# Optimization experiments

Measured on AMD Instinct MI355X. Metric: run time of the kernel, lower is better.

## Reference

```python
import jax, jax.numpy as jnp
import numpy as np

B, S, DM, H, FF, BLOCK, R = 2, 4096, 768, 12, 3072, 64, 3
NB = S // BLOCK  # 64 blocks


def _layer_norm(x, g, b, eps=1e-5):
    mu = jnp.mean(x, -1, keepdims=True)
    var = jnp.var(x, -1, keepdims=True)
    return (x - mu) * jax.lax.rsqrt(var + eps) * g + b


def _bigbird_attn(x, rand_attn, Wq, bq, Wk, bk, Wv, bv):
    b_, s_, dm = x.shape
    h_ = H
    d = dm // h_
    n = s_ // BLOCK
    r = rand_attn.shape[-1]
    scale = 1.0 / np.sqrt(d).astype(np.float32)

    def heads(y):  # [B,S,DM] -> [B,H,n,block,D]
        return y.reshape(b_, s_, h_, d).transpose(0, 2, 1, 3).reshape(b_, h_, n, BLOCK, d)

    qb = heads(x @ Wq + bq)
    kb = heads(x @ Wk + bk)
    vb = heads(x @ Wv + bv)
    k_full = kb.reshape(b_, h_, s_, d)
    v_full = vb.reshape(b_, h_, s_, d)

    # gather random key/value blocks per head: [B,H,n-2,r*block,D]
    gather = jax.vmap(lambda zh, idx: zh[:, idx], in_axes=(1, 0), out_axes=1)
    gk = gather(kb, rand_attn).reshape(b_, h_, n - 2, r * BLOCK, d)
    gv = gather(vb, rand_attn).reshape(b_, h_, n - 2, r * BLOCK, d)

    def attend(q, k, v):
        s = jnp.einsum('...qd,...kd->...qk', q, k) * scale
        a = jax.nn.softmax(s, axis=-1)
        return jnp.einsum('...qk,...kd->...qd', a, v)

    # first block: full attention over all keys
    c_first = attend(qb[:, :, 0], k_full, v_full)

    # second block: blocks 0,1,2 + last block + random blocks
    k2 = jnp.concatenate([kb[:, :, 0], kb[:, :, 1], kb[:, :, 2], kb[:, :, -1], gk[:, :, 0]], axis=2)
    v2 = jnp.concatenate([vb[:, :, 0], vb[:, :, 1], vb[:, :, 2], vb[:, :, -1], gv[:, :, 0]], axis=2)
    c_second = attend(qb[:, :, 1], k2, v2)

    # middle blocks 2..n-3: global-first + 3-block sliding window + random + global-last
    m = n - 4
    qm = qb[:, :, 2:-2]  # [B,H,m,block,D]

    def band(z):  # sliding window of 3 blocks around each middle block
        return jnp.concatenate([z[:, :, 1:-3], z[:, :, 2:-2], z[:, :, 3:-1]], axis=3)

    bc = lambda z: jnp.broadcast_to(z[:, :, None], (b_, h_, m, BLOCK, d))
    km = jnp.concatenate([bc(kb[:, :, 0]), band(kb), gk[:, :, 1:-1], bc(kb[:, :, -1])], axis=3)
    vm = jnp.concatenate([bc(vb[:, :, 0]), band(vb), gv[:, :, 1:-1], bc(vb[:, :, -1])], axis=3)
    c_mid = attend(qm, km, vm)  # [B,H,m,block,D]

    # second-to-last block: block 0 + last three blocks + random blocks
    kp = jnp.concatenate([kb[:, :, 0], kb[:, :, -3], kb[:, :, -2], kb[:, :, -1], gk[:, :, -1]], axis=2)
    vp = jnp.concatenate([vb[:, :, 0], vb[:, :, -3], vb[:, :, -2], vb[:, :, -1], gv[:, :, -1]], axis=2)
    c_pen = attend(qb[:, :, -2], kp, vp)

    # last block: full attention over all keys
    c_last = attend(qb[:, :, -1], k_full, v_full)

    ctx = jnp.concatenate([c_first[:, :, None], c_second[:, :, None], c_mid,
                           c_pen[:, :, None], c_last[:, :, None]], axis=2)
    return ctx.reshape(b_, h_, s_, d).transpose(0, 2, 1, 3).reshape(b_, s_, dm)


def setup_inputs() -> dict:
    key = jax.random.key(0)
    ks = jax.random.split(key, 16)
    p = lambda k, shape: (jax.random.normal(k, shape, jnp.float32) * 0.02)
    return {
        'x': jax.random.normal(ks[0], (B, S, DM), jnp.float32),
        'rand_attn': jax.random.randint(ks[1], (H, NB - 2, R), 0, NB - 2, jnp.int32),
        'Wq': p(ks[2], (DM, DM)), 'bq': jnp.zeros((DM,), jnp.float32),
        'Wk': p(ks[3], (DM, DM)), 'bk': jnp.zeros((DM,), jnp.float32),
        'Wv': p(ks[4], (DM, DM)), 'bv': jnp.zeros((DM,), jnp.float32),
        'ln1_g': jnp.ones((DM,), jnp.float32), 'ln1_b': jnp.zeros((DM,), jnp.float32),
        'W1': p(ks[5], (DM, FF)), 'b1': jnp.zeros((FF,), jnp.float32),
        'W2': p(ks[6], (FF, DM)), 'b2': jnp.zeros((DM,), jnp.float32),
        'ln2_g': jnp.ones((DM,), jnp.float32), 'ln2_b': jnp.zeros((DM,), jnp.float32),
    }


def reference(x, rand_attn, Wq, bq, Wk, bk, Wv, bv, ln1_g, ln1_b, W1, b1, W2, b2, ln2_g, ln2_b):
    attn = _bigbird_attn(x, rand_attn, Wq, bq, Wk, bk, Wv, bv)
    h = _layer_norm(attn + x, ln1_g, ln1_b)  # dropout is identity in eval
    ffn = jax.nn.gelu(h @ W1 + b1, approximate=False) @ W2 + b2
    return _layer_norm(ffn + h, ln2_g, ln2_b)
```

## Files before the change

### kernel.cpp

```cpp
#include <hip/hip_runtime.h>
#include <cmath>


typedef unsigned short bf;
typedef __attribute__((ext_vector_type(8))) short bf16x8;
typedef __attribute__((ext_vector_type(4))) float f32x4;

__device__ __forceinline__ float bf2f(bf u) { return __uint_as_float(((unsigned)u) << 16); }
__device__ __forceinline__ bf f2bf(float f) {
  unsigned x = __float_as_uint(f);
  x += 0x7FFFu + ((x >> 16) & 1u);
  return (bf)(x >> 16);
}

__device__ __forceinline__ void gload16(const bf* g, char* lds) {
  __builtin_amdgcn_global_load_lds(
      (const __attribute__((address_space(1))) void*)g,
      (__attribute__((address_space(3))) void*)lds, 16, 0, 0);
}

__global__ __launch_bounds__(256) void cvt_x_k(const float* __restrict__ X,
                                               bf* __restrict__ xb)
{
  size_t i = ((size_t)blockIdx.x * 256 + threadIdx.x) * 8;
  float4 f0 = *(const float4*)&X[i];
  float4 f1 = *(const float4*)&X[i + 4];
  *(ushort4*)&xb[i]     = make_ushort4(f2bf(f0.x), f2bf(f0.y), f2bf(f0.z), f2bf(f0.w));
  *(ushort4*)&xb[i + 4] = make_ushort4(f2bf(f1.x), f2bf(f1.y), f2bf(f1.z), f2bf(f1.w));
}

__global__ __launch_bounds__(256) void tconv_k(const float* __restrict__ W,
                                               bf* __restrict__ Wt, int K, int N)
{
  __shared__ float tile[64][65];
  const int t = threadIdx.x;
  const int bn = blockIdx.x * 64, bk = blockIdx.y * 64;
  const int r = t >> 2, c0 = (t & 3) * 16;
  #pragma unroll
  for (int i = 0; i < 4; ++i) {
    float4 f = *(const float4*)&W[(size_t)(bk + r) * N + bn + c0 + i * 4];
    tile[r][c0 + i*4 + 0] = f.x; tile[r][c0 + i*4 + 1] = f.y;
    tile[r][c0 + i*4 + 2] = f.z; tile[r][c0 + i*4 + 3] = f.w;
  }
  __syncthreads();
  #pragma unroll
  for (int i = 0; i < 4; ++i) {
    int c = c0 + i * 4;
    ushort4 u = make_ushort4(f2bf(tile[c + 0][r]), f2bf(tile[c + 1][r]),
                             f2bf(tile[c + 2][r]), f2bf(tile[c + 3][r]));
    *(ushort4*)&Wt[(size_t)(bn + r) * K + bk + c] = u;
  }
}

__global__ __launch_bounds__(256) void tconv3_k(const float* __restrict__ Wq,
                                                const float* __restrict__ Wk,
                                                const float* __restrict__ Wv,
                                                bf* __restrict__ Wt)
{
  __shared__ float tile[64][65];
  const float* W = (blockIdx.z == 0) ? Wq : ((blockIdx.z == 1) ? Wk : Wv);
  bf* dst = Wt + (size_t)blockIdx.z * 589824;
  const int t = threadIdx.x;
  const int bn = blockIdx.x * 64, bk = blockIdx.y * 64;
  const int r = t >> 2, c0 = (t & 3) * 16;
  #pragma unroll
  for (int i = 0; i < 4; ++i) {
    float4 f = *(const float4*)&W[(size_t)(bk + r) * 768 + bn + c0 + i * 4];
    tile[r][c0 + i*4 + 0] = f.x; tile[r][c0 + i*4 + 1] = f.y;
    tile[r][c0 + i*4 + 2] = f.z; tile[r][c0 + i*4 + 3] = f.w;
  }
  __syncthreads();
  #pragma unroll
  for (int i = 0; i < 4; ++i) {
    int c = c0 + i * 4;
    ushort4 u = make_ushort4(f2bf(tile[c + 0][r]), f2bf(tile[c + 1][r]),
                             f2bf(tile[c + 2][r]), f2bf(tile[c + 3][r]));
    *(ushort4*)&dst[(size_t)(bn + r) * 768 + bk + c] = u;
  }
}

template <int BN, typename TC>
__global__ __launch_bounds__(256) void gl_gemm_k(
    const bf* __restrict__ A, const bf* __restrict__ Bt,
    const float* __restrict__ bias, TC* __restrict__ C,
    int M, int N, int K, int ldbt, int ep)
{
  constexpr int NJ = BN / 32;
  constexpr int ASZ = 16384;
  constexpr int BSZ = BN * 128;
  __shared__ char smem[2 * (ASZ + BSZ)];
  const int t = threadIdx.x;
  const int bm = blockIdx.y * 128, bn = blockIdx.x * BN;
  const int lane = t & 63, wid = t >> 6;
  const int wm = wid >> 1, wn = wid & 1;
  const int fr = lane & 15, fq = lane >> 4;
  const int lr = lane >> 3;
  const int lksw = (((lane & 7) ^ lr) << 3);

  f32x4 acc[4][NJ];
  #pragma unroll
  for (int i = 0; i < 4; ++i)
    #pragma unroll
    for (int j = 0; j < NJ; ++j) acc[i][j] = (f32x4){0.f, 0.f, 0.f, 0.f};

  auto STAGE = [&](int p, int k0) {
    char* sA = smem + p * (ASZ + BSZ);
    char* sB = sA + ASZ;
    #pragma unroll
    for (int c = 0; c < 4; ++c) {
      int chunk = wid * 4 + c;
      gload16(A + (size_t)(bm + chunk * 8 + lr) * K + k0 + lksw, sA + chunk * 1024);
    }
    #pragma unroll
    for (int c = 0; c < NJ; ++c) {
      int chunk = wid * NJ + c;
      gload16(Bt + (size_t)(bn + chunk * 8 + lr) * ldbt + k0 + lksw, sB + chunk * 1024);
    }
  };

  const int T = K >> 6;
  STAGE(0, 0);
  asm volatile("s_waitcnt vmcnt(0)" ::: "memory");
  __builtin_amdgcn_s_barrier();
  __builtin_amdgcn_sched_barrier(0);
  int cur = 0;
  for (int tt = 0; tt < T; ++tt) {
    if (tt + 1 < T) STAGE(cur ^ 1, (tt + 1) * 64);
    __builtin_amdgcn_sched_barrier(0);
    char* sA = smem + cur * (ASZ + BSZ);
    char* sB = sA + ASZ;
    __builtin_amdgcn_s_setprio(1);
    #pragma unroll
    for (int kk = 0; kk < 2; ++kk) {
      const int kb = kk * 64 + fq * 16;
      bf16x8 a[4], b[NJ];
      #pragma unroll
      for (int i = 0; i < 4; ++i) {
        int row = wm * 64 + i * 16 + fr;
        a[i] = *(const bf16x8*)(sA + row * 128 + (kb ^ ((row & 7) << 4)));
      }
      #pragma unroll
      for (int j = 0; j < NJ; ++j) {
        int col = wn * (BN / 2) + j * 16 + fr;
        b[j] = *(const bf16x8*)(sB + col * 128 + (kb ^ ((col & 7) << 4)));
      }
      #pragma unroll
      for (int i = 0; i < 4; ++i)
        #pragma unroll
        for (int j = 0; j < NJ; ++j)
          acc[i][j] = __builtin_amdgcn_mfma_f32_16x16x32_bf16(a[i], b[j], acc[i][j], 0, 0, 0);
    }
    __builtin_amdgcn_s_setprio(0);
    __builtin_amdgcn_sched_barrier(0);
    asm volatile("s_waitcnt vmcnt(0)" ::: "memory");
    __builtin_amdgcn_s_barrier();
    __builtin_amdgcn_sched_barrier(0);
    cur ^= 1;
  }
  #pragma unroll
  for (int j = 0; j < NJ; ++j) {
    int col = bn + wn * (BN / 2) + j * 16 + fr;
    float bias_v = bias ? bias[col] : 0.f;
    #pragma unroll
    for (int i = 0; i < 4; ++i) {
      int row0 = bm + wm * 64 + i * 16 + fq * 4;
      #pragma unroll
      for (int r = 0; r < 4; ++r) {
        float v = acc[i][j][r] + bias_v;
        if (ep == 1) v = 0.5f * v * (1.0f + erff(v * 0.70710678118654752f));
        if constexpr (sizeof(TC) == 2) C[(size_t)(row0 + r) * N + col] = f2bf(v);
        else                           C[(size_t)(row0 + r) * N + col] = v;
      }
    }
  }
}

__global__ __launch_bounds__(256) void qkv_gl_k(
    const bf* __restrict__ A, const bf* __restrict__ Bt,
    const float* __restrict__ bq, const float* __restrict__ bk,
    const float* __restrict__ bv,
    bf* __restrict__ Qo, bf* __restrict__ Ko, bf* __restrict__ Vo)
{
  constexpr int ASZ = 16384, BSZ = 16384;
  __shared__ char smem[2 * (ASZ + BSZ)];
  const int t = threadIdx.x;
  const int bm = blockIdx.y * 128, bn = blockIdx.x * 128;
  const int lane = t & 63, wid = t >> 6;
  const int wm = wid >> 1, wn = wid & 1;
  const int fr = lane & 15, fq = lane >> 4;
  const int lr = lane >> 3;
  const int lksw = (((lane & 7) ^ lr) << 3);
  const int K = 768;

  f32x4 acc[4][4];
  #pragma unroll
  for (int i = 0; i < 4; ++i)
    #pragma unroll
    for (int j = 0; j < 4; ++j) acc[i][j] = (f32x4){0.f, 0.f, 0.f, 0.f};

  auto STAGE = [&](int p, int k0) {
    char* sA = smem + p * (ASZ + BSZ);
    char* sB = sA + ASZ;
    #pragma unroll
    for (int c = 0; c < 4; ++c) {
      int chunk = wid * 4 + c;
      gload16(A + (size_t)(bm + chunk * 8 + lr) * K + k0 + lksw, sA + chunk * 1024);
    }
    #pragma unroll
    for (int c = 0; c < 4; ++c) {
      int chunk = wid * 4 + c;
      gload16(Bt + (size_t)(bn + chunk * 8 + lr) * K + k0 + lksw, sB + chunk * 1024);
    }
  };

  STAGE(0, 0);
  asm volatile("s_waitcnt vmcnt(0)" ::: "memory");
  __builtin_amdgcn_s_barrier();
  __builtin_amdgcn_sched_barrier(0);
  int cur = 0;
  for (int tt = 0; tt < 12; ++tt) {
    if (tt + 1 < 12) STAGE(cur ^ 1, (tt + 1) * 64);
    __builtin_amdgcn_sched_barrier(0);
    char* sA = smem + cur * (ASZ + BSZ);
    char* sB = sA + ASZ;
    __builtin_amdgcn_s_setprio(1);
    #pragma unroll
    for (int kk = 0; kk < 2; ++kk) {
      const int kb = kk * 64 + fq * 16;
      bf16x8 a[4], b[4];
      #pragma unroll
      for (int i = 0; i < 4; ++i) {
        int row = wm * 64 + i * 16 + fr;
        a[i] = *(const bf16x8*)(sA + row * 128 + (kb ^ ((row & 7) << 4)));
      }
      #pragma unroll
      for (int j = 0; j < 4; ++j) {
        int col = wn * 64 + j * 16 + fr;
        b[j] = *(const bf16x8*)(sB + col * 128 + (kb ^ ((col & 7) << 4)));
      }
      #pragma unroll
      for (int i = 0; i < 4; ++i)
        #pragma unroll
        for (int j = 0; j < 4; ++j)
          acc[i][j] = __builtin_amdgcn_mfma_f32_16x16x32_bf16(a[i], b[j], acc[i][j], 0, 0, 0);
    }
    __builtin_amdgcn_s_setprio(0);
    __builtin_amdgcn_sched_barrier(0);
    asm volatile("s_waitcnt vmcnt(0)" ::: "memory");
    __builtin_amdgcn_s_barrier();
    __builtin_amdgcn_sched_barrier(0);
    cur ^= 1;
  }
  const int seg = bn / 768;
  const int cb  = bn - seg * 768;
  bf* dst = (seg == 0) ? Qo : ((seg == 1) ? Ko : Vo);
  const float* bias = (seg == 0) ? bq : ((seg == 1) ? bk : bv);
  #pragma unroll
  for (int j = 0; j < 4; ++j) {
    int col = cb + wn * 64 + j * 16 + fr;
    float bias_v = bias[col];
    #pragma unroll
    for (int i = 0; i < 4; ++i) {
      int row0 = bm + wm * 64 + i * 16 + fq * 4;
      #pragma unroll
      for (int r = 0; r < 4; ++r)
        dst[(size_t)(row0 + r) * 768 + col] = f2bf(acc[i][j][r] + bias_v);
    }
  }
}

__device__ __forceinline__ void stage_kv(char* bK, char* bVT,
    int kkey, int kd0, int vkey, int w,
    uint4 k0, uint4 k1, uint4 v0, uint4 v1)
{
  const int sw = (kkey & 7) << 4;
  *(uint4*)(bK + kkey * 128 + ((2 * kd0) ^ sw))      = k0;
  *(uint4*)(bK + kkey * 128 + ((2 * kd0 + 16) ^ sw)) = k1;
  union { uint4 q; unsigned short s[8]; } a, c;
  a.q = v0; c.q = v1;
  #pragma unroll
  for (int i = 0; i < 8; ++i) {
    int d = w * 16 + i;
    *(unsigned short*)(bVT + d * 128 + ((2 * vkey) ^ ((d & 7) << 4))) = a.s[i];
  }
  #pragma unroll
  for (int i = 0; i < 8; ++i) {
    int d = w * 16 + 8 + i;
    *(unsigned short*)(bVT + d * 128 + ((2 * vkey) ^ ((d & 7) << 4))) = c.s[i];
  }
}

__global__ __launch_bounds__(256) void attn5_kernel(
    const bf* __restrict__ Q, const bf* __restrict__ K,
    const bf* __restrict__ V, const int* __restrict__ rnd,
    float* __restrict__ ctx, float* __restrict__ part, int nseg)
{
  __shared__ char sQP[8192];
  __shared__ char sKV[2][16384];
  __shared__ int klist[8];
  const int t = threadIdx.x;
  const int lane = t & 63, w = t >> 6;
  const int fr = lane & 15, fq = lane >> 4;
  const int wg = blockIdx.x;
  const int nheavy = 48 * nseg;
  const bool heavy = wg < nheavy;
  int b, h, n, nkb, seg = 0, hidx = 0, segBase = 0;
  if (heavy) {
    hidx = wg / nseg; seg = wg - hidx * nseg;
    n = (hidx & 1) ? 63 : 0;
    int bh = hidx >> 1; h = bh % 12; b = bh / 12;
    nkb = 64 / nseg; segBase = seg * nkb;
  } else {
    int idx = wg - nheavy;
    n = 1 + (idx % 62);
    int bh = idx / 62; h = bh % 12; b = bh / 12;
    nkb = (n == 1 || n == 62) ? 7 : 8;
    if (t == 0) {
      int cnt = 0;
      if (n == 1)       { klist[0]=0; klist[1]=1;  klist[2]=2;  klist[3]=63; cnt=4; }
      else if (n == 62) { klist[0]=0; klist[1]=61; klist[2]=62; klist[3]=63; cnt=4; }
      else              { klist[0]=0; klist[1]=n-1; klist[2]=n; klist[3]=n+1; cnt=4; }
      for (int j = 0; j < 3; ++j) klist[cnt++] = rnd[(h * 62 + (n - 1)) * 3 + j];
      if (n != 1 && n != 62) klist[cnt++] = 63;
    }
  }
  const size_t qbase = ((size_t)b * 4096 + (size_t)n * 64) * 768 + h * 64;

  {
    int row = t >> 2, d0 = (t & 3) * 16;
    const bf* qp = &Q[qbase + (size_t)row * 768 + d0];
    #pragma unroll
    for (int i = 0; i < 2; ++i) {
      int off = row * 128 + ((2 * (d0 + 8 * i)) ^ ((row & 7) << 4));
      *(uint4*)(sQP + off) = *(const uint4*)(qp + 8 * i);
    }
  }
  __syncthreads();
  bf16x8 qf[2];
  {
    int row = w * 16 + fr;
    qf[0] = *(const bf16x8*)(sQP + row * 128 + ((2 * (fq * 8))      ^ ((row & 7) << 4)));
    qf[1] = *(const bf16x8*)(sQP + row * 128 + ((2 * (32 + fq * 8)) ^ ((row & 7) << 4)));
  }

  const int kkey = t >> 2, kd0 = (t & 3) * 16;
  const int vkey = lane;

  uint4 pk0, pk1, pv0, pv1;
  {
    int kb = heavy ? segBase : klist[0];
    size_t kbase = ((size_t)b * 4096 + (size_t)kb * 64) * 768 + h * 64;
    const bf* kp = &K[kbase + (size_t)kkey * 768 + kd0];
    pk0 = *(const uint4*)kp;  pk1 = *(const uint4*)(kp + 8);
    const bf* vp = &V[kbase + (size_t)vkey * 768 + w * 16];
    pv0 = *(const uint4*)vp;  pv1 = *(const uint4*)(vp + 8);
  }
  stage_kv(sKV[0], sKV[0] + 8192, kkey, kd0, vkey, w, pk0, pk1, pv0, pv1);

  float m_r[4] = {-1e30f, -1e30f, -1e30f, -1e30f};
  float l_r[4] = {0.f, 0.f, 0.f, 0.f};
  f32x4 acc_o[4];
  #pragma unroll
  for (int j = 0; j < 4; ++j) acc_o[j] = (f32x4){0.f, 0.f, 0.f, 0.f};

  for (int ib = 0; ib < nkb; ++ib) {
    char* bK  = sKV[ib & 1];
    char* bVT = bK + 8192;
    const bool pfv = (ib + 1 < nkb);
    if (pfv) {
      int kb = heavy ? (segBase + ib + 1) : klist[ib + 1];
      size_t kbase = ((size_t)b * 4096 + (size_t)kb * 64) * 768 + h * 64;
      const bf* kp = &K[kbase + (size_t)kkey * 768 + kd0];
      pk0 = *(const uint4*)kp;  pk1 = *(const uint4*)(kp + 8);
      const bf* vp = &V[kbase + (size_t)vkey * 768 + w * 16];
      pv0 = *(const uint4*)vp;  pv1 = *(const uint4*)(vp + 8);
    }
    __syncthreads();
    f32x4 s4[4];
    #pragma unroll
    for (int j = 0; j < 4; ++j) s4[j] = (f32x4){0.f, 0.f, 0.f, 0.f};
    __builtin_amdgcn_s_setprio(1);
    #pragma unroll
    for (int kk = 0; kk < 2; ++kk) {
      #pragma unroll
      for (int j = 0; j < 4; ++j) {
        int key = j * 16 + fr;
        bf16x8 kf = *(const bf16x8*)(bK + key * 128 + ((2 * (kk * 32 + fq * 8)) ^ ((key & 7) << 4)));
        s4[j] = __builtin_amdgcn_mfma_f32_16x16x32_bf16(qf[kk], kf, s4[j], 0, 0, 0);
      }
    }
    __builtin_amdgcn_s_setprio(0);
    #pragma unroll
    for (int j = 0; j < 4; ++j) s4[j] *= 0.125f;
    float c_r[4];
    #pragma unroll
    for (int r = 0; r < 4; ++r) {
      float mx = fmaxf(fmaxf(s4[0][r], s4[1][r]), fmaxf(s4[2][r], s4[3][r]));
      #pragma unroll
      for (int m = 1; m < 16; m <<= 1) mx = fmaxf(mx, __shfl_xor(mx, m, 64));
      float mn = fmaxf(mx, m_r[r]);
      float c  = __expf(m_r[r] - mn);
      float p0 = __expf(s4[0][r] - mn), p1 = __expf(s4[1][r] - mn);
      float p2 = __expf(s4[2][r] - mn), p3 = __expf(s4[3][r] - mn);
      s4[0][r] = p0; s4[1][r] = p1; s4[2][r] = p2; s4[3][r] = p3;
      float sum = p0 + p1 + p2 + p3;
      #pragma unroll
      for (int m = 1; m < 16; m <<= 1) sum += __shfl_xor(sum, m, 64);
      l_r[r] = l_r[r] * c + sum;
      m_r[r] = mn;
      c_r[r] = c;
    }
    #pragma unroll
    for (int j = 0; j < 4; ++j)
      #pragma unroll
      for (int r = 0; r < 4; ++r) acc_o[j][r] *= c_r[r];
    #pragma unroll
    for (int r = 0; r < 4; ++r) {
      int prow = w * 16 + fq * 4 + r;
      int rs = prow * 128, sw = (prow & 7) << 4;
      #pragma unroll
      for (int j = 0; j < 4; ++j)
        *(unsigned short*)(sQP + rs + ((2 * (j * 16 + fr)) ^ sw)) = f2bf(s4[j][r]);
    }
    if (pfv)
      stage_kv(sKV[(ib & 1) ^ 1], sKV[(ib & 1) ^ 1] + 8192, kkey, kd0, vkey, w,
               pk0, pk1, pv0, pv1);
    __builtin_amdgcn_s_setprio(1);
    #pragma unroll
    for (int kk = 0; kk < 2; ++kk) {
      int prow = w * 16 + fr;
      bf16x8 pf8 = *(const bf16x8*)(sQP + prow * 128 + ((2 * (kk * 32 + fq * 8)) ^ ((prow & 7) << 4)));
      #pragma unroll
      for (int j = 0; j < 4; ++j) {
        int col = j * 16 + fr;
        bf16x8 vf = *(const bf16x8*)(bVT + col * 128 + ((2 * (kk * 32 + fq * 8)) ^ ((col & 7) << 4)));
        acc_o[j] = __builtin_amdgcn_mfma_f32_16x16x32_bf16(pf8, vf, acc_o[j], 0, 0, 0);
      }
    }
    __builtin_amdgcn_s_setprio(0);
  }
  if (heavy && nseg > 1) {
    float* pb = part + ((size_t)hidx * nseg + seg) * 4224;
    int row0 = w * 16 + fq * 4;
    #pragma unroll
    for (int r = 0; r < 4; ++r) {
      int row = row0 + r;
      if (fr == 0) { pb[4096 + row] = m_r[r]; pb[4160 + row] = l_r[r]; }
      #pragma unroll
      for (int j = 0; j < 4; ++j)
        pb[row * 64 + j * 16 + fr] = acc_o[j][r];
    }
  } else {
    int row0 = w * 16 + fq * 4;
    #pragma unroll
    for (int r = 0; r < 4; ++r) {
      float inv = 1.f / l_r[r];
      size_t rowoff = qbase + (size_t)(row0 + r) * 768;
      #pragma unroll
      for (int j = 0; j < 4; ++j)
        ctx[rowoff + j * 16 + fr] = acc_o[j][r] * inv;
    }
  }
}

__global__ __launch_bounds__(256) void attn_combine_k(
    const float* __restrict__ part, float* __restrict__ ctx)
{
  const int hidx = blockIdx.x;
  const int t = threadIdx.x;
  const int n = (hidx & 1) ? 63 : 0;
  const int bh = hidx >> 1;
  const int h = bh % 12, b = bh / 12;
  const size_t qbase = ((size_t)b * 4096 + (size_t)n * 64) * 768 + h * 64;
  const int r = t >> 2, d0 = (t & 3) * 16;
  const float* pb = part + (size_t)hidx * 8 * 4224;
  float mi[8], li[8], m = -1e30f;
  #pragma unroll
  for (int i = 0; i < 8; ++i) {
    mi[i] = pb[i * 4224 + 4096 + r];
    li[i] = pb[i * 4224 + 4160 + r];
    m = fmaxf(m, mi[i]);
  }
  float w8[8], L = 0.f;
  #pragma unroll
  for (int i = 0; i < 8; ++i) { w8[i] = __expf(mi[i] - m); L += li[i] * w8[i]; }
  float inv = 1.f / L;
  #pragma unroll
  for (int dd = 0; dd < 4; ++dd) {
    int d = d0 + dd * 4;
    float4 o = {0.f, 0.f, 0.f, 0.f};
    #pragma unroll
    for (int i = 0; i < 8; ++i) {
      float4 p = *(const float4*)&pb[i * 4224 + r * 64 + d];
      o.x = fmaf(w8[i], p.x, o.x); o.y = fmaf(w8[i], p.y, o.y);
      o.z = fmaf(w8[i], p.z, o.z); o.w = fmaf(w8[i], p.w, o.w);
    }
    o.x *= inv; o.y *= inv; o.z *= inv; o.w *= inv;
    *(float4*)&ctx[qbase + (size_t)r * 768 + d] = o;
  }
}

template <typename TR, typename TO>
__global__ __launch_bounds__(256) void ln_kernel(
    const float* __restrict__ a, const TR* __restrict__ res,
    const float* __restrict__ g, const float* __restrict__ bb,
    TO* __restrict__ out)
{
  const int row = blockIdx.x, t = threadIdx.x;
  __shared__ float buf[768];
  __shared__ float rs[4], rss[4];
  const size_t base = (size_t)row * 768;
  float s = 0.f, ss = 0.f;
  for (int c = t; c < 768; c += 256) {
    float rv;
    if constexpr (sizeof(TR) == 2) rv = bf2f(res[base + c]);
    else                           rv = res[base + c];
    float v = a[base + c] + rv;
    buf[c] = v;
    s += v;
    ss = fmaf(v, v, ss);
  }
  #pragma unroll
  for (int off = 32; off > 0; off >>= 1) {
    s  += __shfl_down(s, off, 64);
    ss += __shfl_down(ss, off, 64);
  }
  if ((t & 63) == 0) { rs[t >> 6] = s; rss[t >> 6] = ss; }
  __syncthreads();
  float S  = rs[0] + rs[1] + rs[2] + rs[3];
  float SS = rss[0] + rss[1] + rss[2] + rss[3];
  float mu  = S * (1.f / 768.f);
  float var = SS * (1.f / 768.f) - mu * mu;
  float inv = rsqrtf(var + 1e-5f);
  for (int c = t; c < 768; c += 256) {
    float v = (buf[c] - mu) * inv * g[c] + bb[c];
    if constexpr (sizeof(TO) == 2) out[base + c] = f2bf(v);
    else                           out[base + c] = v;
  }
}

extern "C" void kernel_launch(void* const* d_in, const int* in_sizes, int n_in,
                              void* d_out, int out_size, void* d_ws, size_t ws_size,
                              hipStream_t stream)
{
  const float* x   = (const float*)d_in[0];
  const int*   rnd = (const int*)d_in[1];
  const float* Wq  = (const float*)d_in[2];
  const float* bq  = (const float*)d_in[3];
  const float* Wk  = (const float*)d_in[4];
  const float* bk  = (const float*)d_in[5];
  const float* Wv  = (const float*)d_in[6];
  const float* bv  = (const float*)d_in[7];
  const float* g1  = (const float*)d_in[8];
  const float* be1 = (const float*)d_in[9];
  const float* W1  = (const float*)d_in[10];
  const float* b1  = (const float*)d_in[11];
  const float* W2  = (const float*)d_in[12];
  const float* b2  = (const float*)d_in[13];
  const float* g2  = (const float*)d_in[14];
  const float* be2 = (const float*)d_in[15];
  float* out = (float*)d_out;

  char* W = (char*)d_ws;
  bf* w1t   = (bf*)(W);
  bf* w2t   = (bf*)(W + 4718592);
  bf* Kb    = (bf*)(W + 9437184);
  bf* wqkv  = (bf*)(W + 22020096);
  bf* xb    = (bf*)(W + 25559040);
  bf* Qb    = (bf*)(W + 38141952);
  bf* Vb    = (bf*)(W + 50724864);
  float* part = (float*)(W + 63307776);
  bf* f1    = (bf*)(W + 22020096);
  bf* h1    = Kb;
  float* ctx = out;
  float* f2  = out;

  dim3 blk(256);
  cvt_x_k<<<dim3(3072), blk, 0, stream>>>(x, xb);
  tconv3_k<<<dim3(12, 12, 3), blk, 0, stream>>>(Wq, Wk, Wv, wqkv);
  tconv_k<<<dim3(48, 12), blk, 0, stream>>>(W1, w1t,  768, 3072);
  tconv_k<<<dim3(12, 48), blk, 0, stream>>>(W2, w2t, 3072,  768);
  qkv_gl_k<<<dim3(18, 64), blk, 0, stream>>>(xb, wqkv, bq, bk, bv, Qb, Kb, Vb);
  attn5_kernel<<<dim3(48 * 8 + 2 * 12 * 62), blk, 0, stream>>>(
      Qb, Kb, Vb, rnd, ctx, part, 8);
  attn_combine_k<<<dim3(48), blk, 0, stream>>>(part, ctx);
  ln_kernel<float, bf><<<dim3(8192), blk, 0, stream>>>(ctx, x, g1, be1, h1);
  gl_gemm_k<128, bf><<<dim3(24, 64), blk, 0, stream>>>(
      h1, w1t, b1, f1, 8192, 3072, 768, 768, 1);
  gl_gemm_k<128, float><<<dim3(6, 64), blk, 0, stream>>>(
      f1, w2t, b2, f2, 8192, 768, 3072, 3072, 0);
  ln_kernel<bf, float><<<dim3(8192), blk, 0, stream>>>(f2, h1, g2, be2, out);
}
```

Baseline: 280.3 us.

## Add 256x256-tile 8-wave pipelined GEMM for FFN up-projection with fused GELU

Replaces the 128x128-tile GEMM for the first FFN matmul with a new kernel that uses 512 threads and 256x256 output tiles. It double-buffers 64-wide K slices in 128 KB of LDS, staged in half-tile pieces interleaved with MFMA work under explicit vmcnt waits and barriers. The larger tile raises operand reuse per LDS byte and overlaps global loads with compute, and the epilogue keeps the bias and erf GELU. The cost is heavy register and LDS use, so only one block fits per CU, and the grid shrinks to 384 blocks, which may not fill every CU evenly.

```diff
diff --git a/kernel.cpp b/kernel.cpp
--- a/kernel.cpp
+++ b/kernel.cpp
@@ -76,6 +76,116 @@
     ushort4 u = make_ushort4(f2bf(tile[c + 0][r]), f2bf(tile[c + 1][r]),
                              f2bf(tile[c + 2][r]), f2bf(tile[c + 3][r]));
     *(ushort4*)&dst[(size_t)(bn + r) * 768 + bk + c] = u;
+  }
+}
+
+__global__ __launch_bounds__(512) void gemm8_k(
+    const bf* __restrict__ A, const bf* __restrict__ Bt,
+    const float* __restrict__ bias, bf* __restrict__ C,
+    int M, int N, int K, int ldbt)
+{
+  __shared__ char smem[131072];
+  const int t = threadIdx.x;
+  const int bm = blockIdx.y * 256, bn = blockIdx.x * 256;
+  const int lane = t & 63, wid = t >> 6;
+  const int wm = wid >> 2, wn = wid & 3;
+  const int fr = lane & 15, fq = lane >> 4;
+
+  f32x4 acc[8][4];
+  #pragma unroll
+  for (int i = 0; i < 8; ++i)
+    #pragma unroll
+    for (int q = 0; q < 4; ++q) acc[i][q] = (f32x4){0.f, 0.f, 0.f, 0.f};
+
+  auto STAGE_HALF = [&](int d, int which, int kt) {
+    char* base = smem + d * 65536 + ((which >= 2) ? 32768 : 0);
+    int h = which & 1;
+    const bf* P = (which >= 2) ? Bt : A;
+    int ld  = (which >= 2) ? ldbt : K;
+    int rc0 = ((which >= 2) ? bn : bm) + h * 128;
+    int k0  = kt * 64;
+    #pragma unroll
+    for (int c = 0; c < 2; ++c) {
+      int idx = c * 512 + t;
+      int rl = idx >> 3, ks = idx & 7;
+      gload16(P + (size_t)(rc0 + rl) * ld + k0 + ((ks ^ (rl & 7)) << 3),
+              base + h * 16384 + (c * 512 + wid * 64) * 16);
+    }
+  };
+
+  const int T = K >> 6;
+  STAGE_HALF(0, 0, 0); STAGE_HALF(0, 1, 0); STAGE_HALF(0, 2, 0); STAGE_HALF(0, 3, 0);
+  asm volatile("s_waitcnt vmcnt(2)" ::: "memory");
+  __builtin_amdgcn_s_barrier();
+  __builtin_amdgcn_sched_barrier(0);
+
+  bf16x8 ac[2][8];
+
+  for (int i2 = 0; i2 < T; i2 += 2) {
+    #pragma unroll
+    for (int p = 0; p < 8; ++p) {
+      constexpr int P8 = 1;  (void)P8;
+      const int d = p >> 2;
+      const int q = p & 3;
+      if (p < 4) { if (i2 + 1 < T) STAGE_HALF(1, p, i2 + 1); }
+      else       { if (i2 + 2 < T) STAGE_HALF(0, p - 4, i2 + 2); }
+      __builtin_amdgcn_sched_barrier(0);
+      char* sA = smem + d * 65536;
+      char* sB = sA + 32768;
+      if (q == 0) {
+        #pragma unroll
+        for (int kh = 0; kh < 2; ++kh)
+          #pragma unroll
+          for (int i = 0; i < 8; ++i) {
+            int row = wm * 128 + i * 16 + fr;
+            ac[kh][i] = *(const bf16x8*)(sA + row * 128 +
+                          ((kh * 64 + fq * 16) ^ ((row & 7) << 4)));
+          }
+      }
+      bf16x8 bfr[2];
+      #pragma unroll
+      for (int kh = 0; kh < 2; ++kh) {
+        int col = q * 64 + wn * 16 + fr;
+        bfr[kh] = *(const bf16x8*)(sB + col * 128 +
+                      ((kh * 64 + fq * 16) ^ ((col & 7) << 4)));
+      }
+      __builtin_amdgcn_s_setprio(1);
+      #pragma unroll
+      for (int kh = 0; kh < 2; ++kh)
+        #pragma unroll
+        for (int i = 0; i < 8; ++i)
+          acc[i][q] = __builtin_amdgcn_mfma_f32_16x16x32_bf16(ac[kh][i], bfr[kh], acc[i][q], 0, 0, 0);
+      __builtin_amdgcn_s_setprio(0);
+      __builtin_amdgcn_sched_barrier(0);
+      if (p == 1) {
+        asm volatile("s_waitcnt vmcnt(4)" ::: "memory");
+      } else if (p == 3) {
+        asm volatile("s_waitcnt vmcnt(2)" ::: "memory");
+      } else if (p == 5) {
+        if (i2 + 2 < T) { asm volatile("s_waitcnt vmcnt(4)" ::: "memory"); }
+        else            { asm volatile("s_waitcnt vmcnt(0)" ::: "memory"); }
+      } else if (p == 7) {
+        if (i2 + 2 < T) { asm volatile("s_waitcnt vmcnt(2)" ::: "memory"); }
+        else            { asm volatile("s_waitcnt vmcnt(0)" ::: "memory"); }
+      }
+      __builtin_amdgcn_s_barrier();
+      __builtin_amdgcn_sched_barrier(0);
+    }
+  }
+  #pragma unroll
+  for (int q = 0; q < 4; ++q) {
+    int col = bn + q * 64 + wn * 16 + fr;
+    float bias_v = bias[col];
+    #pragma unroll
+    for (int i = 0; i < 8; ++i) {
+      int row0 = bm + wm * 128 + i * 16 + fq * 4;
+      #pragma unroll
+      for (int r = 0; r < 4; ++r) {
+        float v = acc[i][q][r] + bias_v;
+        v = 0.5f * v * (1.0f + erff(v * 0.70710678118654752f));
+        C[(size_t)(row0 + r) * N + col] = f2bf(v);
+      }
+    }
   }
 }
 
@@ -585,8 +695,8 @@
       Qb, Kb, Vb, rnd, ctx, part, 8);
   attn_combine_k<<<dim3(48), blk, 0, stream>>>(part, ctx);
   ln_kernel<float, bf><<<dim3(8192), blk, 0, stream>>>(ctx, x, g1, be1, h1);
-  gl_gemm_k<128, bf><<<dim3(24, 64), blk, 0, stream>>>(
-      h1, w1t, b1, f1, 8192, 3072, 768, 768, 1);
+  gemm8_k<<<dim3(12, 32), dim3(512), 0, stream>>>(
+      h1, w1t, b1, f1, 8192, 3072, 768, 768);
   gl_gemm_k<128, float><<<dim3(6, 64), blk, 0, stream>>>(
       f1, w2t, b2, f2, 8192, 768, 3072, 3072, 0);
   ln_kernel<bf, float><<<dim3(8192), blk, 0, stream>>>(f2, h1, g2, be2, out);
```

New measurement: 284.2 us. No clear change (+1.4%).
